# Optimization experiments

Measured on AMD Instinct MI355X. Metric: run time of the kernel, lower is better.

Reference implementation:

```python
import jax, jax.numpy as jnp
import numpy as np

T, B, D, H = 110, 256, 512, 512
EPS = 1e-9


def _forward(a, v, l, qmask, umask, mu_a, mu_v, mu_l, shifta, shiftv,
             turna, turnb, W1, b1, W2, b2):
    Tcur = a.shape[0]
    # ca = mu * (cos(a) + i sin(a)) = mu * exp(i a)
    ca = mu_a[:Tcur] * jnp.exp(1j * a)          # (T,B,D) complex64
    cv = mu_v[:Tcur] * jnp.exp(1j * v)
    cl = mu_l[:Tcur] * jnp.exp(1j * l)
    # phase shift of a and v streams, then sum into lav
    features = cl + ca * jnp.exp(1j * shifta) + cv * jnp.exp(1j * shiftv)  # (T,B,D)

    # --- step 0 (special-cased in the original loop) ---
    temp0 = features[0]                          # (B,D) complex
    qa0 = qmask[0][:, 0:1]                       # (B,1)
    qb0 = qmask[0][:, 1:2]
    ones = jnp.ones_like(temp0) * (1.0 + 1.0j)   # pA=pB=1+1j initial state
    pA0 = (1.0 - qa0) * ones + qa0 * temp0
    pB0 = (1.0 - qb0) * ones + qb0 * temp0

    # --- steps 1..T-1 as a fused scan over time ---
    def step(carry, xs):
        pA, pB = carry
        f, qm, ta, tb = xs                       # f:(B,D) cplx, qm:(B,2), ta/tb:(1,D)
        qa = qm[:, 0:1]
        qb = qm[:, 1:2]
        turn = qa * (pA * jnp.exp(1j * ta)) + qb * (pB * jnp.exp(1j * tb))
        # torch: turn.where(turn==0, turn/(abs+eps)) -> keep 0 where 0, else normalize
        turn = jnp.where(turn == 0, turn, turn / (jnp.abs(turn) + EPS))
        temp = f + turn
        pA = (1.0 - qa) * pA + qa * temp
        pB = (1.0 - qb) * pB + qb * temp
        return (pA, pB), temp

    (_, _), temps = jax.lax.scan(
        step, (pA0, pB0),
        (features[1:], qmask[1:], turna[1:Tcur], turnb[1:Tcur]))

    feats = jnp.concatenate([temp0[None], temps], axis=0)  # (T,B,D) complex
    fr, fi = feats.real, feats.imag
    f1r = fr @ W1.T + b1
    f1i = fi @ W1.T + b1
    f2r = fr @ W2.T + b2
    f2i = fi @ W2.T + b2
    xr = f1r - f2i
    xi = f1i + f2r
    return xr + xi                               # (T,B,H) float32


def setup_inputs() -> dict:
    key = jax.random.key(0)
    ks = jax.random.split(key, 12)
    a = jax.random.normal(ks[0], (T, B, D), jnp.float32)
    v = jax.random.normal(ks[1], (T, B, D), jnp.float32)
    l = jax.random.normal(ks[2], (T, B, D), jnp.float32)
    spk = jax.random.randint(ks[3], (T, B), 0, 2)
    qmask = jax.nn.one_hot(spk, 2, dtype=jnp.float32)      # (T,B,2)
    umask = jnp.ones((T, B), jnp.float32)                  # unused by forward
    mu_a = jnp.ones((110, 1, 1), jnp.float32)
    mu_v = jnp.ones((110, 1, 1), jnp.float32)
    mu_l = jnp.ones((110, 1, 1), jnp.float32)
    shifta = jax.random.normal(ks[4], (1, 1, D), jnp.float32)
    shiftv = jax.random.normal(ks[5], (1, 1, D), jnp.float32)
    turna = jax.random.uniform(ks[6], (110, 1, D), jnp.float32)
    turnb = jax.random.uniform(ks[7], (110, 1, D), jnp.float32)
    W1 = jax.random.normal(ks[8], (H, D), jnp.float32) * 0.02
    b1 = jnp.zeros((H,), jnp.float32)
    W2 = jax.random.normal(ks[9], (H, D), jnp.float32) * 0.02
    b2 = jnp.zeros((H,), jnp.float32)
    return {"a": a, "v": v, "l": l, "qmask": qmask, "umask": umask,
            "mu_a": mu_a, "mu_v": mu_v, "mu_l": mu_l,
            "shifta": shifta, "shiftv": shiftv,
            "turna": turna, "turnb": turnb,
            "W1": W1, "b1": b1, "W2": W2, "b2": b2,
            "dia_len": T}


def reference(a, v, l, qmask, umask, mu_a, mu_v, mu_l, shifta, shiftv,
              turna, turnb, W1, b1, W2, b2, dia_len):
    return _forward(a, v, l, qmask, umask, mu_a, mu_v, mu_l,
                    shifta, shiftv, turna, turnb, W1, b1, W2, b2)
```

## Files before the change

### kernel.cpp

```cpp
#include <hip/hip_runtime.h>

#define T_DIM 110
#define B_DIM 256
#define D_DIM 512
#define H_DIM 512
#define K_CAT 1024
#define M_DIM (T_DIM * B_DIM)
#define BD    (B_DIM * D_DIM)
#define EPSV 1e-9f

typedef float f32x4 __attribute__((ext_vector_type(4)));
typedef short bf16x8 __attribute__((ext_vector_type(8)));

static __device__ __forceinline__ unsigned short f2bf(float f) {
    unsigned u = __builtin_bit_cast(unsigned, f);
    u += 0x7fffu + ((u >> 16) & 1u);
    return (unsigned short)(u >> 16);
}

__global__ __launch_bounds__(256) void prep_w_kernel(
    const float* __restrict__ W1, const float* __restrict__ b1,
    const float* __restrict__ W2,
    unsigned short* __restrict__ Bt,
    float* __restrict__ bias2)
{
    int i = blockIdx.x * 256 + threadIdx.x;
    if (i < H_DIM) bias2[i] = 2.0f * b1[i];
    if (i >= H_DIM * K_CAT) return;
    int h = i / K_CAT;
    int k = i % K_CAT;
    int j = k >> 1;
    float w = (k & 1) ? (W1[h * D_DIM + j] - W2[h * D_DIM + j])
                      : (W1[h * D_DIM + j] + W2[h * D_DIM + j]);
    Bt[i] = f2bf(w);
}

__global__ __launch_bounds__(256) void prep_tt_kernel(
    const float* __restrict__ turna, const float* __restrict__ turnb,
    float4* __restrict__ TT)
{
    int i = blockIdx.x * 256 + threadIdx.x;
    if (i >= T_DIM * D_DIM) return;
    float s1, c1, s2, c2;
    __sincosf(turna[i], &s1, &c1);
    __sincosf(turnb[i], &s2, &c2);
    TT[i] = make_float4(c1, s1, c2, s2);
}

__global__ __launch_bounds__(256) void feat_scan_kernel(
    const float* __restrict__ a, const float* __restrict__ v,
    const float* __restrict__ l, const float* __restrict__ qmask,
    const float* __restrict__ mu_a, const float* __restrict__ mu_v,
    const float* __restrict__ mu_l,
    const float* __restrict__ shifta, const float* __restrict__ shiftv,
    const float4* __restrict__ TT,
    unsigned int* __restrict__ A32)
{
    __shared__ float qm_s[T_DIM], mua_s[T_DIM], muv_s[T_DIM], mul_s[T_DIM];
    const int tx = threadIdx.x;
    const int b  = blockIdx.x >> 1;
    const int d  = ((blockIdx.x & 1) << 8) + tx;
    if (tx < T_DIM) {
        qm_s[tx]  = qmask[(size_t)(tx * B_DIM + b) * 2];
        mua_s[tx] = mu_a[tx];
        muv_s[tx] = mu_v[tx];
        mul_s[tx] = mu_l[tx];
    }
    const float sa = shifta[d];
    const float sv = shiftv[d];
    __syncthreads();

    const size_t gbase = (size_t)b * D_DIM + d;

    float  s0a = a[gbase],                 s0v = v[gbase],
           s0l = l[gbase];
    float4 s0t = TT[d];
    float  s1a = a[(size_t)1 * BD + gbase], s1v = v[(size_t)1 * BD + gbase],
           s1l = l[(size_t)1 * BD + gbase];
    float4 s1t = TT[1 * D_DIM + d];
    float  s2a = a[(size_t)2 * BD + gbase], s2v = v[(size_t)2 * BD + gbase],
           s2l = l[(size_t)2 * BD + gbase];
    float4 s2t = TT[2 * D_DIM + d];
    float  s3a = a[(size_t)3 * BD + gbase], s3v = v[(size_t)3 * BD + gbase],
           s3l = l[(size_t)3 * BD + gbase];
    float4 s3t = TT[3 * D_DIM + d];

    float pAr = 1.f, pAi = 1.f, pBr = 1.f, pBi = 1.f;

#define ITER(tt_, SA_, SV_, SL_, ST_)                                          \
    {                                                                          \
        const int t_ = (tt_);                                                  \
        const float qa = qm_s[t_], ma = mua_s[t_],                             \
                    mv = muv_s[t_], ml = mul_s[t_];                            \
        float sA, cA, sV, cV, sL, cL;                                          \
        __sincosf(SA_ + sa, &sA, &cA);                                         \
        __sincosf(SV_ + sv, &sV, &cV);                                         \
        __sincosf(SL_,      &sL, &cL);                                         \
        float fr = ml * cL + ma * cA + mv * cV;                                \
        float fi = ml * sL + ma * sA + mv * sV;                                \
        const bool isA = qa > 0.5f;                                            \
        const float cp = isA ? ST_.x : ST_.z;                                  \
        const float sp = isA ? ST_.y : ST_.w;                                  \
        const float pr = isA ? pAr : pBr;                                      \
        const float pi = isA ? pAi : pBi;                                      \
        const float tr = pr * cp - pi * sp;                                    \
        const float ti = pr * sp + pi * cp;                                    \
        const float gate = (t_ == 0) ? 0.0f : 1.0f;                            \
        const float m2 = fmaxf(tr * tr + ti * ti, 1e-30f);                     \
        const float inv = gate * __builtin_amdgcn_rsqf(m2);                    \
        fr += tr * inv;                                                        \
        fi += ti * inv;                                                        \
        pAr = isA ? fr : pAr;  pAi = isA ? fi : pAi;                           \
        pBr = isA ? pBr : fr;  pBi = isA ? pBi : fi;                           \
        A32[(size_t)(t_ * B_DIM + b) * (K_CAT / 2) + d] =                      \
            (unsigned)f2bf(fr) | ((unsigned)f2bf(fi) << 16);                   \
                   \
        const int tnx = (t_ + 4 < T_DIM) ? t_ + 4 : T_DIM - 1;                 \
        SA_ = a[(size_t)tnx * BD + gbase];                                     \
        SV_ = v[(size_t)tnx * BD + gbase];                                     \
        SL_ = l[(size_t)tnx * BD + gbase];                                     \
        ST_ = TT[(size_t)tnx * D_DIM + d];                                     \
                  \
        __builtin_amdgcn_sched_barrier(0x387);                                 \
    }

    for (int tb = 0; tb < 108; tb += 4) {
        ITER(tb,     s0a, s0v, s0l, s0t)
        ITER(tb + 1, s1a, s1v, s1l, s1t)
        ITER(tb + 2, s2a, s2v, s2l, s2t)
        ITER(tb + 3, s3a, s3v, s3l, s3t)
    }
    ITER(108, s0a, s0v, s0l, s0t)
    ITER(109, s1a, s1v, s1l, s1t)
#undef ITER
}

#define BM 128
#define BN 128
#define BK 64

__global__ __launch_bounds__(256) void gemm_kernel(
    const unsigned short* __restrict__ A,
    const unsigned short* __restrict__ Bt,
    const float* __restrict__ bias2,
    float* __restrict__ C)
{
    __shared__ __align__(16) unsigned short As[BM * BK];
    __shared__ __align__(16) unsigned short Bs[BN * BK];

    const int tid = threadIdx.x;
    const int wave = tid >> 6;
    const int lane = tid & 63;
    const int wr = wave >> 1;
    const int wc = wave & 1;
    const int m0 = blockIdx.x * BM;
    const int n0 = blockIdx.y * BN;
    const int lrow = lane & 15;
    const int lk8 = (lane >> 4) * 8;

    const int srow = wave * 32;
    const int lrow8 = lane >> 3;
    const int lchunk = lane & 7;

    f32x4 acc[4][4] = {};

    for (int k0 = 0; k0 < K_CAT; k0 += BK) {
        #pragma unroll
        for (int c = 0; c < 4; ++c) {
            const int row = srow + c * 8 + lrow8;
            {
                const unsigned short* gp = A + (size_t)(m0 + row) * K_CAT + k0 + lchunk * 8;
                unsigned short* lp = As + (srow + c * 8) * BK + lane * 8;
                __builtin_amdgcn_global_load_lds(
                    (const __attribute__((address_space(1))) unsigned int*)gp,
                    (__attribute__((address_space(3))) unsigned int*)lp,
                    16, 0, 0);
            }
            {
                const unsigned short* gp = Bt + (size_t)(n0 + row) * K_CAT + k0 + lchunk * 8;
                unsigned short* lp = Bs + (srow + c * 8) * BK + lane * 8;
                __builtin_amdgcn_global_load_lds(
                    (const __attribute__((address_space(1))) unsigned int*)gp,
                    (__attribute__((address_space(3))) unsigned int*)lp,
                    16, 0, 0);
            }
        }
        __syncthreads();

        bf16x8 af[4][2], bfv[4][2];
        #pragma unroll
        for (int m = 0; m < 4; ++m)
            #pragma unroll
            for (int kk = 0; kk < 2; ++kk)
                af[m][kk] = *reinterpret_cast<const bf16x8*>(
                    &As[(wr * 64 + m * 16 + lrow) * BK + kk * 32 + lk8]);
        #pragma unroll
        for (int n = 0; n < 4; ++n)
            #pragma unroll
            for (int kk = 0; kk < 2; ++kk)
                bfv[n][kk] = *reinterpret_cast<const bf16x8*>(
                    &Bs[(wc * 64 + n * 16 + lrow) * BK + kk * 32 + lk8]);

        #pragma unroll
        for (int kk = 0; kk < 2; ++kk)
            #pragma unroll
            for (int m = 0; m < 4; ++m)
                #pragma unroll
                for (int n = 0; n < 4; ++n)
                    acc[m][n] = __builtin_amdgcn_mfma_f32_16x16x32_bf16(
                        af[m][kk], bfv[n][kk], acc[m][n], 0, 0, 0);
        __syncthreads();
    }

    const int rbase = m0 + wr * 64 + (lane >> 4) * 4;
    const int cbase = n0 + wc * 64;
    #pragma unroll
    for (int n = 0; n < 4; ++n) {
        const int col = cbase + n * 16 + lrow;
        const float bv = bias2[col];
        #pragma unroll
        for (int m = 0; m < 4; ++m) {
            const int row0 = rbase + m * 16;
            #pragma unroll
            for (int r = 0; r < 4; ++r) {
                C[(size_t)(row0 + r) * H_DIM + col] = acc[m][n][r] + bv;
            }
        }
    }
}

extern "C" void kernel_launch(void* const* d_in, const int* in_sizes, int n_in,
                              void* d_out, int out_size, void* d_ws, size_t ws_size,
                              hipStream_t stream) {
    const float* a      = (const float*)d_in[0];
    const float* v      = (const float*)d_in[1];
    const float* l      = (const float*)d_in[2];
    const float* qmask  = (const float*)d_in[3];
    const float* mu_a   = (const float*)d_in[5];
    const float* mu_v   = (const float*)d_in[6];
    const float* mu_l   = (const float*)d_in[7];
    const float* shifta = (const float*)d_in[8];
    const float* shiftv = (const float*)d_in[9];
    const float* turna  = (const float*)d_in[10];
    const float* turnb  = (const float*)d_in[11];
    const float* W1     = (const float*)d_in[12];
    const float* b1     = (const float*)d_in[13];
    const float* W2     = (const float*)d_in[14];
    float* out = (float*)d_out;

    char* ws = (char*)d_ws;
    unsigned short* Afeat = (unsigned short*)ws;
    size_t offB  = (size_t)M_DIM * K_CAT * sizeof(unsigned short);
    unsigned short* Bt = (unsigned short*)(ws + offB);
    size_t offBias = offB + (size_t)H_DIM * K_CAT * sizeof(unsigned short);
    float* bias2 = (float*)(ws + offBias);
    size_t offTT = offBias + 4096;
    float4* TT = (float4*)(ws + offTT);

    prep_w_kernel<<<(H_DIM * K_CAT + 255) / 256, 256, 0, stream>>>(W1, b1, W2, Bt, bias2);
    prep_tt_kernel<<<(T_DIM * D_DIM + 255) / 256, 256, 0, stream>>>(turna, turnb, TT);
    feat_scan_kernel<<<B_DIM * 2, 256, 0, stream>>>(
        a, v, l, qmask, mu_a, mu_v, mu_l, shifta, shiftv, TT, (unsigned int*)Afeat);
    dim3 grid(M_DIM / BM, H_DIM / BN);
    gemm_kernel<<<grid, 256, 0, stream>>>(Afeat, Bt, bias2, out);
}
```

Measured before the change: 112.0 us.

## Split scan into independent per-speaker chains and swap GEMM grid order

The scan is split into two independent chains, one per speaker, each run by its own block. Each block builds a list of the timesteps its speaker owns and walks only those. This halves the serial dependency length per block and doubles the number of blocks. The GEMM grid is also transposed so that consecutive blocks share the same A row tile, which may improve cache reuse. The cost is a serial list build by one thread and more scattered timestep loads.

```diff
diff --git a/kernel.cpp b/kernel.cpp
--- a/kernel.cpp
+++ b/kernel.cpp
@@ -7,7 +7,6 @@
 #define K_CAT 1024
 #define M_DIM (T_DIM * B_DIM)
 #define BD    (B_DIM * D_DIM)
-#define EPSV 1e-9f
 
 typedef float f32x4 __attribute__((ext_vector_type(4)));
 typedef short bf16x8 __attribute__((ext_vector_type(8)));
@@ -53,86 +52,97 @@
     const float* __restrict__ mu_a, const float* __restrict__ mu_v,
     const float* __restrict__ mu_l,
     const float* __restrict__ shifta, const float* __restrict__ shiftv,
-    const float4* __restrict__ TT,
+    const float2* __restrict__ TT2,
     unsigned int* __restrict__ A32)
 {
-    __shared__ float qm_s[T_DIM], mua_s[T_DIM], muv_s[T_DIM], mul_s[T_DIM];
-    const int tx = threadIdx.x;
-    const int b  = blockIdx.x >> 1;
-    const int d  = ((blockIdx.x & 1) << 8) + tx;
+    const int bid   = blockIdx.x;
+    const int b     = bid >> 2;
+    const int dhalf = (bid >> 1) & 1;
+    const int chain = bid & 1;
+    const int tx    = threadIdx.x;
+    const int d     = (dhalf << 8) + tx;
+
+    __shared__ float mua_s[T_DIM], muv_s[T_DIM], mul_s[T_DIM], qtmp[T_DIM];
+    __shared__ short tlist[T_DIM];
+    __shared__ int nt_s;
+
     if (tx < T_DIM) {
-        qm_s[tx]  = qmask[(size_t)(tx * B_DIM + b) * 2];
+        qtmp[tx]  = qmask[(size_t)(tx * B_DIM + b) * 2];
         mua_s[tx] = mu_a[tx];
         muv_s[tx] = mu_v[tx];
         mul_s[tx] = mu_l[tx];
     }
+    __syncthreads();
+    if (tx == 0) {
+        int n = 0;
+        for (int t = 0; t < T_DIM; ++t) {
+            const bool own = (chain == 0) ? (qtmp[t] > 0.5f) : !(qtmp[t] > 0.5f);
+            if (own) tlist[n++] = (short)t;
+        }
+        nt_s = n;
+    }
+    __syncthreads();
+    const int nt = nt_s;
+    if (nt == 0) return;
+
     const float sa = shifta[d];
     const float sv = shiftv[d];
-    __syncthreads();
-
     const size_t gbase = (size_t)b * D_DIM + d;
 
-    float  s0a = a[gbase],                 s0v = v[gbase],
-           s0l = l[gbase];
-    float4 s0t = TT[d];
-    float  s1a = a[(size_t)1 * BD + gbase], s1v = v[(size_t)1 * BD + gbase],
-           s1l = l[(size_t)1 * BD + gbase];
-    float4 s1t = TT[1 * D_DIM + d];
-    float  s2a = a[(size_t)2 * BD + gbase], s2v = v[(size_t)2 * BD + gbase],
-           s2l = l[(size_t)2 * BD + gbase];
-    float4 s2t = TT[2 * D_DIM + d];
-    float  s3a = a[(size_t)3 * BD + gbase], s3v = v[(size_t)3 * BD + gbase],
-           s3l = l[(size_t)3 * BD + gbase];
-    float4 s3t = TT[3 * D_DIM + d];
-
-    float pAr = 1.f, pAi = 1.f, pBr = 1.f, pBi = 1.f;
-
-#define ITER(tt_, SA_, SV_, SL_, ST_)                                          \
+#define LOADSLOT(TS_, SA_, SV_, SL_, SC_, jj_)                                 \
+    { const int j_ = (jj_); const int jc = j_ < nt ? j_ : nt - 1;              \
+      TS_ = (int)tlist[jc];                                                    \
+      SA_ = a[(size_t)TS_ * BD + gbase];                                       \
+      SV_ = v[(size_t)TS_ * BD + gbase];                                       \
+      SL_ = l[(size_t)TS_ * BD + gbase];                                       \
+      SC_ = TT2[((size_t)TS_ * D_DIM + d) * 2 + chain]; }
+
+    int    t0, t1, t2, t3;
+    float  a0, v0, l0, a1, v1, l1, a2, v2, l2, a3, v3, l3;
+    float2 c0, c1, c2, c3;
+    LOADSLOT(t0, a0, v0, l0, c0, 0)
+    LOADSLOT(t1, a1, v1, l1, c1, 1)
+    LOADSLOT(t2, a2, v2, l2, c2, 2)
+    LOADSLOT(t3, a3, v3, l3, c3, 3)
+
+    float pr = 1.f, pi = 1.f;
+
+#define ITER(ii_, TS_, SA_, SV_, SL_, SC_)                                     \
     {                                                                          \
-        const int t_ = (tt_);                                                  \
-        const float qa = qm_s[t_], ma = mua_s[t_],                             \
-                    mv = muv_s[t_], ml = mul_s[t_];                            \
+        const int i_ = (ii_);                                                  \
+        const bool act = i_ < nt;                           \
+        const float ma = mua_s[TS_], mv = muv_s[TS_], ml = mul_s[TS_];         \
         float sA, cA, sV, cV, sL, cL;                                          \
         __sincosf(SA_ + sa, &sA, &cA);                                         \
         __sincosf(SV_ + sv, &sV, &cV);                                         \
         __sincosf(SL_,      &sL, &cL);                                         \
         float fr = ml * cL + ma * cA + mv * cV;                                \
         float fi = ml * sL + ma * sA + mv * sV;                                \
-        const bool isA = qa > 0.5f;                                            \
-        const float cp = isA ? ST_.x : ST_.z;                                  \
-        const float sp = isA ? ST_.y : ST_.w;                                  \
-        const float pr = isA ? pAr : pBr;                                      \
-        const float pi = isA ? pAi : pBi;                                      \
-        const float tr = pr * cp - pi * sp;                                    \
-        const float ti = pr * sp + pi * cp;                                    \
-        const float gate = (t_ == 0) ? 0.0f : 1.0f;                            \
+        const float tr = pr * SC_.x - pi * SC_.y;                              \
+        const float ti = pr * SC_.y + pi * SC_.x;                              \
+        const float gate = (TS_ == 0) ? 0.0f : 1.0f;                           \
         const float m2 = fmaxf(tr * tr + ti * ti, 1e-30f);                     \
         const float inv = gate * __builtin_amdgcn_rsqf(m2);                    \
         fr += tr * inv;                                                        \
         fi += ti * inv;                                                        \
-        pAr = isA ? fr : pAr;  pAi = isA ? fi : pAi;                           \
-        pBr = isA ? pBr : fr;  pBi = isA ? pBi : fi;                           \
-        A32[(size_t)(t_ * B_DIM + b) * (K_CAT / 2) + d] =                      \
-            (unsigned)f2bf(fr) | ((unsigned)f2bf(fi) << 16);                   \
-                   \
-        const int tnx = (t_ + 4 < T_DIM) ? t_ + 4 : T_DIM - 1;                 \
-        SA_ = a[(size_t)tnx * BD + gbase];                                     \
-        SV_ = v[(size_t)tnx * BD + gbase];                                     \
-        SL_ = l[(size_t)tnx * BD + gbase];                                     \
-        ST_ = TT[(size_t)tnx * D_DIM + d];                                     \
-                  \
-        __builtin_amdgcn_sched_barrier(0x387);                                 \
-    }
-
-    for (int tb = 0; tb < 108; tb += 4) {
-        ITER(tb,     s0a, s0v, s0l, s0t)
-        ITER(tb + 1, s1a, s1v, s1l, s1t)
-        ITER(tb + 2, s2a, s2v, s2l, s2t)
-        ITER(tb + 3, s3a, s3v, s3l, s3t)
-    }
-    ITER(108, s0a, s0v, s0l, s0t)
-    ITER(109, s1a, s1v, s1l, s1t)
+        if (act) {                                                             \
+            pr = fr; pi = fi;                                                  \
+            A32[(size_t)(TS_ * B_DIM + b) * (K_CAT / 2) + d] =                 \
+                (unsigned)f2bf(fr) | ((unsigned)f2bf(fi) << 16);               \
+        }                                                                      \
+        LOADSLOT(TS_, SA_, SV_, SL_, SC_, i_ + 4)                              \
+        __builtin_amdgcn_sched_barrier(0x387);           \
+    }
+
+    const int ntp = (nt + 3) & ~3;
+    for (int i = 0; i < ntp; i += 4) {
+        ITER(i + 0, t0, a0, v0, l0, c0)
+        ITER(i + 1, t1, a1, v1, l1, c1)
+        ITER(i + 2, t2, a2, v2, l2, c2)
+        ITER(i + 3, t3, a3, v3, l3, c3)
+    }
 #undef ITER
+#undef LOADSLOT
 }
 
 #define BM 128
@@ -153,8 +163,8 @@
     const int lane = tid & 63;
     const int wr = wave >> 1;
     const int wc = wave & 1;
-    const int m0 = blockIdx.x * BM;
-    const int n0 = blockIdx.y * BN;
+    const int m0 = blockIdx.y * BM;
+    const int n0 = blockIdx.x * BN;
     const int lrow = lane & 15;
     const int lk8 = (lane >> 4) * 8;
 
@@ -259,8 +269,9 @@
 
     prep_w_kernel<<<(H_DIM * K_CAT + 255) / 256, 256, 0, stream>>>(W1, b1, W2, Bt, bias2);
     prep_tt_kernel<<<(T_DIM * D_DIM + 255) / 256, 256, 0, stream>>>(turna, turnb, TT);
-    feat_scan_kernel<<<B_DIM * 2, 256, 0, stream>>>(
-        a, v, l, qmask, mu_a, mu_v, mu_l, shifta, shiftv, TT, (unsigned int*)Afeat);
-    dim3 grid(M_DIM / BM, H_DIM / BN);
+    feat_scan_kernel<<<B_DIM * 4, 256, 0, stream>>>(
+        a, v, l, qmask, mu_a, mu_v, mu_l, shifta, shiftv,
+        (const float2*)TT, (unsigned int*)Afeat);
+    dim3 grid(H_DIM / BN, M_DIM / BM);
     gemm_kernel<<<grid, 256, 0, stream>>>(Afeat, Bt, bias2, out);
 }
```

New measurement: 126.3 us. +12.8%, slower.
